# Performance work log

Hardware: AMD Instinct MI355X
Metric: run time of the kernel (lower is better)

## Reference

```python
import jax, jax.numpy as jnp
import numpy as np

B, S, D = 1, 2048, 4096
H = 32
HD = D // H  # 128
THETA = 10000.0


def _precompute_freqs_cis(dim, end, dtype=jnp.float32):
    freqs = 1.0 / THETA ** (jnp.arange(0, dim, 2)[: dim // 2].astype(dtype) / dim)
    t = jnp.arange(end)
    freqs = jnp.outer(t, freqs).astype(dtype)
    return jnp.complex64(jnp.cos(freqs) + 1j * jnp.sin(freqs))  # [end, dim//2]


def _apply_rotary_emb(xq, xk, freqs_cis, dtype=jnp.float32):
    # xq, xk: [b, s, h, hd]; freqs_cis: [1, s, hd//2] complex
    rq = xq.astype(jnp.float32).reshape(*xq.shape[:-1], -1, 2)
    rk = xk.astype(jnp.float32).reshape(*xk.shape[:-1], -1, 2)
    xq_ = jax.lax.complex(rq[..., 0], rq[..., 1])
    xk_ = jax.lax.complex(rk[..., 0], rk[..., 1])
    fc = jnp.reshape(freqs_cis, (*freqs_cis.shape[:2], 1, *freqs_cis.shape[2:]))  # [1,s,1,hd//2]
    xq_out = xq_ * fc
    xk_out = xk_ * fc
    xq_out = jnp.stack((jnp.real(xq_out), jnp.imag(xq_out)), axis=-1).reshape(*xq_out.shape[:-1], -1)
    xk_out = jnp.stack((jnp.real(xk_out), jnp.imag(xk_out)), axis=-1).reshape(*xk_out.shape[:-1], -1)
    return xq_out.astype(dtype), xk_out.astype(dtype)


def setup_inputs() -> dict:
    key = jax.random.key(0)
    k1, k2, k3 = jax.random.split(key, 3)
    scale = 1.0 / np.sqrt(D)
    return {
        "hidden_states": jax.random.normal(k1, (B, S, D), dtype=jnp.float32),
        "w_qkv_kernel": jax.random.normal(k2, (D, 3 * D), dtype=jnp.float32) * scale,
        "wo_kernel": jax.random.normal(k3, (D, D), dtype=jnp.float32) * scale,
    }


def reference(hidden_states, w_qkv_kernel, wo_kernel):
    b, s, d = hidden_states.shape
    qkv = hidden_states @ w_qkv_kernel  # [b, s, 3d]
    q, k, v = jnp.split(qkv, 3, -1)
    q = q.reshape(b, s, H, HD)
    k = k.reshape(b, s, H, HD)
    v = v.reshape(b, s, H, HD)
    freq = _precompute_freqs_cis(HD, S)[:s].reshape(1, s, -1)
    q, k = _apply_rotary_emb(q, k, freq)
    attn = jnp.einsum("bqhd,bkhd->bhqk", q, k)
    attn = attn * (1.0 / np.sqrt(HD))
    attn = jax.nn.softmax(attn, axis=-1)
    out = jnp.einsum("bhqk,bkhd->bqhd", attn, v).reshape(b, s, d)
    return out @ wo_kernel
```

## Files before the change

### kernel.cpp

```cpp
#include <hip/hip_runtime.h>
#include <cstdint>

#define S_LEN   2048
#define D_MODEL 4096
#define NHEAD   32
#define HDIM    128
#define LDQKV   12288

typedef __bf16 bf16x8 __attribute__((ext_vector_type(8)));
typedef float  f32x4  __attribute__((ext_vector_type(4)));
typedef unsigned short u16;
typedef unsigned int   u32;

union U16x8 { u16 u[8]; uint4 v; };

static __device__ __forceinline__ u16 f2b(float f) {
  u32 u = __builtin_bit_cast(u32, f);
  u += 0x7fffu + ((u >> 16) & 1u);
  return (u16)(u >> 16);
}
static __device__ __forceinline__ float b2f(u16 h) {
  u32 u = ((u32)h) << 16;
  return __builtin_bit_cast(float, u);
}

#define GLOAD_LDS16(gp, lp)                                                   \
  __builtin_amdgcn_global_load_lds(                                           \
      (const __attribute__((address_space(1))) unsigned int*)(gp),            \
      (__attribute__((address_space(3))) unsigned int*)(lp), 16, 0, 0)

__global__ __launch_bounds__(256) void convert_f32_bf16(
    const float* __restrict__ in, u16* __restrict__ out) {
  size_t i = (size_t)blockIdx.x * 256 + threadIdx.x;
  const float4* p = (const float4*)in;
  float4 a = p[2 * i], b = p[2 * i + 1];
  U16x8 r;
  r.u[0] = f2b(a.x); r.u[1] = f2b(a.y); r.u[2] = f2b(a.z); r.u[3] = f2b(a.w);
  r.u[4] = f2b(b.x); r.u[5] = f2b(b.y); r.u[6] = f2b(b.z); r.u[7] = f2b(b.w);
  *(uint4*)(out + 8 * i) = r.v;
}

__global__ __launch_bounds__(256) void tconv(
    const float* __restrict__ in, u16* __restrict__ out, int R, int C) {
  __shared__ __align__(16) u16 tile[64][72];
  const int r0 = blockIdx.y * 64, c0 = blockIdx.x * 64;
  const int tid = threadIdx.x;
  const int tr = tid >> 4, tc = (tid & 15) * 4;
#pragma unroll
  for (int p = 0; p < 4; ++p) {
    float4 v = *(const float4*)(in + (size_t)(r0 + p * 16 + tr) * C + c0 + tc);
    u16* t = &tile[p * 16 + tr][tc];
    t[0] = f2b(v.x); t[1] = f2b(v.y); t[2] = f2b(v.z); t[3] = f2b(v.w);
  }
  __syncthreads();
  const int oc = tid >> 3, os = (tid & 7) * 8;
#pragma unroll
  for (int p = 0; p < 2; ++p) {
    U16x8 u;
#pragma unroll
    for (int j = 0; j < 8; ++j) u.u[j] = tile[os + j][p * 32 + oc];
    *(uint4*)(out + (size_t)(c0 + p * 32 + oc) * R + r0 + os) = u.v;
  }
}

template <typename OutT>
__global__ __launch_bounds__(256) void gemm_bt(
    const u16* __restrict__ A, const u16* __restrict__ Bt, OutT* __restrict__ C,
    int M, int N, int K) {
  __shared__ __align__(16) u16 As[128 * 64];
  __shared__ __align__(16) u16 Bs[128 * 64];
  const int tid = threadIdx.x;
  const int lane = tid & 63, wave = tid >> 6;
  const int lane15 = lane & 15, quad = lane >> 4;
  const int wm = (wave >> 1) * 64, wn = (wave & 1) * 64;
  const size_t bm = (size_t)blockIdx.y * 128, bn = (size_t)blockIdx.x * 128;
  const int sreg_row = lane >> 3;
  const int schunk = lane & 7;

  f32x4 acc[4][4] = {};

  for (int k0 = 0; k0 < K; k0 += 64) {
#pragma unroll
    for (int i = 0; i < 4; ++i) {
      const int reg = wave * 4 + i;
      const int row = reg * 8 + sreg_row;
      const int gc = schunk ^ (row & 7);
      GLOAD_LDS16(A + (bm + row) * (size_t)K + k0 + gc * 8, &As[reg * 512]);
      GLOAD_LDS16(Bt + (bn + row) * (size_t)K + k0 + gc * 8, &Bs[reg * 512]);
    }
    __syncthreads();
#pragma unroll
    for (int kk = 0; kk < 64; kk += 32) {
      const int cb = kk >> 3;
      bf16x8 af[4], bfr[4];
#pragma unroll
      for (int mt = 0; mt < 4; ++mt) {
        const int row = wm + mt * 16 + lane15;
        af[mt] = *(const bf16x8*)&As[row * 64 + (((cb + quad) ^ (lane15 & 7)) * 8)];
      }
#pragma unroll
      for (int nt = 0; nt < 4; ++nt) {
        const int row = wn + nt * 16 + lane15;
        bfr[nt] = *(const bf16x8*)&Bs[row * 64 + (((cb + quad) ^ (lane15 & 7)) * 8)];
      }
#pragma unroll
      for (int mt = 0; mt < 4; ++mt)
#pragma unroll
        for (int nt = 0; nt < 4; ++nt)
          acc[mt][nt] = __builtin_amdgcn_mfma_f32_16x16x32_bf16(
              af[mt], bfr[nt], acc[mt][nt], 0, 0, 0);
    }
    __syncthreads();
  }
#pragma unroll
  for (int mt = 0; mt < 4; ++mt)
#pragma unroll
    for (int r = 0; r < 4; ++r) {
      size_t row = bm + wm + mt * 16 + quad * 4 + r;
#pragma unroll
      for (int nt = 0; nt < 4; ++nt) {
        size_t col = bn + wn + nt * 16 + lane15;
        float v = acc[mt][nt][r];
        if constexpr (sizeof(OutT) == 2) C[row * N + col] = (OutT)f2b(v);
        else                             C[row * N + col] = v;
      }
    }
}

__global__ __launch_bounds__(256) void rope_kernel(u16* __restrict__ qkv) {
  int idx = blockIdx.x * 256 + threadIdx.x;
  int s = idx >> 11;
  int p = idx & 2047;
  int h = p >> 6, j = p & 63;
  float freq = exp2f(-(float)j * 0.20762050593046015f);
  float ang = (float)s * freq;
  float sn, cs;
  sincosf(ang, &sn, &cs);
  size_t base = (size_t)s * LDQKV + h * HDIM + 2 * j;
  u32 q = *(const u32*)(qkv + base);
  float q0 = b2f((u16)(q & 0xffff)), q1 = b2f((u16)(q >> 16));
  u32 qo = (u32)f2b(q0 * cs - q1 * sn) | ((u32)f2b(q0 * sn + q1 * cs) << 16);
  *(u32*)(qkv + base) = qo;
  u32 k = *(const u32*)(qkv + base + D_MODEL);
  float k0 = b2f((u16)(k & 0xffff)), k1 = b2f((u16)(k >> 16));
  u32 ko = (u32)f2b(k0 * cs - k1 * sn) | ((u32)f2b(k0 * sn + k1 * cs) << 16);
  *(u32*)(qkv + base + D_MODEL) = ko;
}

__global__ __launch_bounds__(256) void transpose_v(
    const u16* __restrict__ qkv, u16* __restrict__ vt) {
  __shared__ __align__(16) u16 tile[64][72];
  const int s0 = blockIdx.x * 64, d0 = blockIdx.y * 64, h = blockIdx.z;
  const int tid = threadIdx.x;
  const int tr = tid >> 3, tc = (tid & 7) * 8;
#pragma unroll
  for (int p = 0; p < 2; ++p)
    *(uint4*)&tile[p * 32 + tr][tc] =
        *(const uint4*)(qkv + (size_t)(s0 + p * 32 + tr) * LDQKV + 2 * D_MODEL +
                        h * HDIM + d0 + tc);
  __syncthreads();
  const int dd = tid >> 3, ss = (tid & 7) * 8;
#pragma unroll
  for (int p = 0; p < 2; ++p) {
    U16x8 u;
#pragma unroll
    for (int j = 0; j < 8; ++j) u.u[j] = tile[ss + j][p * 32 + dd];
    *(uint4*)(vt + (size_t)h * HDIM * S_LEN + (size_t)(d0 + p * 32 + dd) * S_LEN +
              s0 + ss) = u.v;
  }
}

__global__ __launch_bounds__(256) void attn_kernel(
    const u16* __restrict__ qkv, const u16* __restrict__ vt, u16* __restrict__ ctx) {
  __shared__ __align__(16) u16 Ks[64 * 136];
  __shared__ __align__(16) u16 Vs[128 * 72];
  __shared__ __align__(16) u16 Ps[4][16 * 72];
  const int h = blockIdx.y, qt = blockIdx.x;
  const int tid = threadIdx.x;
  const int lane = tid & 63, wave = tid >> 6;
  const int lane15 = lane & 15, quad = lane >> 4;
  const int q0 = qt * 64 + wave * 16;

  bf16x8 aq[4];
#pragma unroll
  for (int kt = 0; kt < 4; ++kt)
    aq[kt] = *(const bf16x8*)(qkv + (size_t)(q0 + lane15) * LDQKV + h * HDIM +
                              kt * 32 + quad * 8);

  f32x4 o[8] = {};
  float lsum[4] = {0.f, 0.f, 0.f, 0.f};

  const int krow = tid >> 4, kcol = (tid & 15) * 8;
  const int vrow = tid >> 3, vcol = (tid & 7) * 8;
  const float cexp = 0.12751879523243985f;

  for (int kv0 = 0; kv0 < S_LEN; kv0 += 64) {
#pragma unroll
    for (int p = 0; p < 4; ++p)
      *(uint4*)&Ks[(p * 16 + krow) * 136 + kcol] =
          *(const uint4*)(qkv + (size_t)(kv0 + p * 16 + krow) * LDQKV + D_MODEL +
                          h * HDIM + kcol);
#pragma unroll
    for (int p = 0; p < 4; ++p)
      *(uint4*)&Vs[(p * 32 + vrow) * 72 + vcol] =
          *(const uint4*)(vt + (size_t)h * HDIM * S_LEN +
                          (size_t)(p * 32 + vrow) * S_LEN + kv0 + vcol);
    __syncthreads();

    f32x4 sf[4] = {};
#pragma unroll
    for (int nt = 0; nt < 4; ++nt)
#pragma unroll
      for (int kt = 0; kt < 4; ++kt) {
        bf16x8 bk = *(const bf16x8*)&Ks[(nt * 16 + lane15) * 136 + kt * 32 + quad * 8];
        sf[nt] = __builtin_amdgcn_mfma_f32_16x16x32_bf16(aq[kt], bk, sf[nt], 0, 0, 0);
      }

#pragma unroll
    for (int nt = 0; nt < 4; ++nt)
#pragma unroll
      for (int r = 0; r < 4; ++r) {
        float pv = exp2f(sf[nt][r] * cexp);
        lsum[r] += pv;
        Ps[wave][(quad * 4 + r) * 72 + nt * 16 + lane15] = f2b(pv);
      }

#pragma unroll
    for (int kt2 = 0; kt2 < 2; ++kt2) {
      bf16x8 ap = *(const bf16x8*)&Ps[wave][lane15 * 72 + kt2 * 32 + quad * 8];
#pragma unroll
      for (int nt2 = 0; nt2 < 8; ++nt2) {
        bf16x8 bv = *(const bf16x8*)&Vs[(nt2 * 16 + lane15) * 72 + kt2 * 32 + quad * 8];
        o[nt2] = __builtin_amdgcn_mfma_f32_16x16x32_bf16(ap, bv, o[nt2], 0, 0, 0);
      }
    }
    __syncthreads();
  }

#pragma unroll
  for (int r = 0; r < 4; ++r) {
    float l = lsum[r];
    l += __shfl_xor(l, 1);
    l += __shfl_xor(l, 2);
    l += __shfl_xor(l, 4);
    l += __shfl_xor(l, 8);
    float inv = 1.0f / l;
    size_t row = q0 + quad * 4 + r;
#pragma unroll
    for (int nt2 = 0; nt2 < 8; ++nt2)
      ctx[row * D_MODEL + h * HDIM + nt2 * 16 + lane15] = f2b(o[nt2][r] * inv);
  }
}

extern "C" void kernel_launch(void* const* d_in, const int* in_sizes, int n_in,
                              void* d_out, int out_size, void* d_ws, size_t ws_size,
                              hipStream_t stream) {
  const float* hs    = (const float*)d_in[0];
  const float* w_qkv = (const float*)d_in[1];
  const float* wo    = (const float*)d_in[2];
  float* out = (float*)d_out;

  char* w = (char*)d_ws;
  u16* hsb   = (u16*)(w);
  u16* wqkvT = (u16*)(w + (16u  << 20));
  u16* woT   = (u16*)(w + (112u << 20));
  u16* qkvb  = (u16*)(w + (144u << 20));
  u16* vt    = (u16*)(w + (192u << 20));
  u16* ctx   = hsb;

  convert_f32_bf16<<<4096, 256, 0, stream>>>(hs, hsb);
  tconv<<<dim3(12288 / 64, 4096 / 64), 256, 0, stream>>>(w_qkv, wqkvT, 4096, 12288);
  tconv<<<dim3(4096 / 64, 4096 / 64), 256, 0, stream>>>(wo, woT, 4096, 4096);

  gemm_bt<u16><<<dim3(12288 / 128, 2048 / 128), 256, 0, stream>>>(
      hsb, wqkvT, qkvb, 2048, 12288, 4096);

  rope_kernel<<<(S_LEN * 2048) / 256, 256, 0, stream>>>(qkvb);
  transpose_v<<<dim3(32, 2, 32), 256, 0, stream>>>(qkvb, vt);
  attn_kernel<<<dim3(32, 32), 256, 0, stream>>>(qkvb, vt, ctx);

  gemm_bt<float><<<dim3(4096 / 128, 2048 / 128), 256, 0, stream>>>(
      ctx, woT, out, 2048, 4096, 4096);
}
```

Measured before the change: 934.1 us.

## Double query rows per attention wave, use direct-to-LDS swizzled K/V loads

Each attention wave now processes 32 query rows instead of 16, so every K and V fragment read from LDS feeds two MFMAs, and the grid shrinks to 16x32 blocks. K/V tiles are loaded with global_load_lds into XOR-swizzled unpadded LDS layouts, which avoids register staging and bank conflicts. The transpose kernels switch to a 65-wide padded tile with scalar LDS writes, and rope uses fast __sinf/__cosf. Costs include higher register pressure, fewer blocks in flight, and reduced accuracy of sin/cos for large angles.

```diff
diff --git a/kernel.cpp b/kernel.cpp
--- a/kernel.cpp
+++ b/kernel.cpp
@@ -42,7 +42,7 @@
 
 __global__ __launch_bounds__(256) void tconv(
     const float* __restrict__ in, u16* __restrict__ out, int R, int C) {
-  __shared__ __align__(16) u16 tile[64][72];
+  __shared__ u16 tile[64][65];
   const int r0 = blockIdx.y * 64, c0 = blockIdx.x * 64;
   const int tid = threadIdx.x;
   const int tr = tid >> 4, tc = (tid & 15) * 4;
@@ -134,8 +134,7 @@
   int h = p >> 6, j = p & 63;
   float freq = exp2f(-(float)j * 0.20762050593046015f);
   float ang = (float)s * freq;
-  float sn, cs;
-  sincosf(ang, &sn, &cs);
+  float sn = __sinf(ang), cs = __cosf(ang);
   size_t base = (size_t)s * LDQKV + h * HDIM + 2 * j;
   u32 q = *(const u32*)(qkv + base);
   float q0 = b2f((u16)(q & 0xffff)), q1 = b2f((u16)(q >> 16));
@@ -149,15 +148,19 @@
 
 __global__ __launch_bounds__(256) void transpose_v(
     const u16* __restrict__ qkv, u16* __restrict__ vt) {
-  __shared__ __align__(16) u16 tile[64][72];
+  __shared__ u16 tile[64][65];
   const int s0 = blockIdx.x * 64, d0 = blockIdx.y * 64, h = blockIdx.z;
   const int tid = threadIdx.x;
   const int tr = tid >> 3, tc = (tid & 7) * 8;
 #pragma unroll
-  for (int p = 0; p < 2; ++p)
-    *(uint4*)&tile[p * 32 + tr][tc] =
-        *(const uint4*)(qkv + (size_t)(s0 + p * 32 + tr) * LDQKV + 2 * D_MODEL +
-                        h * HDIM + d0 + tc);
+  for (int p = 0; p < 2; ++p) {
+    U16x8 u;
+    u.v = *(const uint4*)(qkv + (size_t)(s0 + p * 32 + tr) * LDQKV + 2 * D_MODEL +
+                          h * HDIM + d0 + tc);
+    u16* t = &tile[p * 32 + tr][tc];
+#pragma unroll
+    for (int j = 0; j < 8; ++j) t[j] = u.u[j];
+  }
   __syncthreads();
   const int dd = tid >> 3, ss = (tid & 7) * 8;
 #pragma unroll
@@ -170,86 +173,106 @@
   }
 }
 
-__global__ __launch_bounds__(256) void attn_kernel(
+__global__ __launch_bounds__(256, 2) void attn_kernel(
     const u16* __restrict__ qkv, const u16* __restrict__ vt, u16* __restrict__ ctx) {
-  __shared__ __align__(16) u16 Ks[64 * 136];
-  __shared__ __align__(16) u16 Vs[128 * 72];
-  __shared__ __align__(16) u16 Ps[4][16 * 72];
+  __shared__ __align__(16) u16 Ks[64 * 128];
+  __shared__ __align__(16) u16 Vs[128 * 64];
+  __shared__ __align__(16) u16 Ps[4][32 * 72];
   const int h = blockIdx.y, qt = blockIdx.x;
   const int tid = threadIdx.x;
   const int lane = tid & 63, wave = tid >> 6;
   const int lane15 = lane & 15, quad = lane >> 4;
-  const int q0 = qt * 64 + wave * 16;
-
-  bf16x8 aq[4];
-#pragma unroll
-  for (int kt = 0; kt < 4; ++kt)
-    aq[kt] = *(const bf16x8*)(qkv + (size_t)(q0 + lane15) * LDQKV + h * HDIM +
-                              kt * 32 + quad * 8);
-
-  f32x4 o[8] = {};
-  float lsum[4] = {0.f, 0.f, 0.f, 0.f};
-
-  const int krow = tid >> 4, kcol = (tid & 15) * 8;
-  const int vrow = tid >> 3, vcol = (tid & 7) * 8;
+  const int q0 = qt * 128 + wave * 32;
+
+  bf16x8 aq[2][4];
+#pragma unroll
+  for (int mi = 0; mi < 2; ++mi)
+#pragma unroll
+    for (int kt = 0; kt < 4; ++kt)
+      aq[mi][kt] = *(const bf16x8*)(qkv + (size_t)(q0 + mi * 16 + lane15) * LDQKV +
+                                    h * HDIM + kt * 32 + quad * 8);
+
+  f32x4 o[2][8] = {};
+  float lsum[2][4] = {};
+
+  const int krow_off = wave * 16 + (lane >> 4);
+  const int kslot = lane & 15;
+  const int vrow_off = wave * 32 + (lane >> 3);
+  const int vslot = lane & 7;
+  const u16* kbase = qkv + D_MODEL + h * HDIM;
+  const u16* vbase = vt + (size_t)h * HDIM * S_LEN;
   const float cexp = 0.12751879523243985f;
 
   for (int kv0 = 0; kv0 < S_LEN; kv0 += 64) {
 #pragma unroll
-    for (int p = 0; p < 4; ++p)
-      *(uint4*)&Ks[(p * 16 + krow) * 136 + kcol] =
-          *(const uint4*)(qkv + (size_t)(kv0 + p * 16 + krow) * LDQKV + D_MODEL +
-                          h * HDIM + kcol);
-#pragma unroll
-    for (int p = 0; p < 4; ++p)
-      *(uint4*)&Vs[(p * 32 + vrow) * 72 + vcol] =
-          *(const uint4*)(vt + (size_t)h * HDIM * S_LEN +
-                          (size_t)(p * 32 + vrow) * S_LEN + kv0 + vcol);
+    for (int i = 0; i < 4; ++i) {
+      const int krow = krow_off + i * 4;
+      const int kgc = kslot ^ (krow & 7);
+      GLOAD_LDS16(kbase + (size_t)(kv0 + krow) * LDQKV + kgc * 8,
+                  &Ks[(wave * 16 + i * 4) * 128]);
+      const int vrow = vrow_off + i * 8;
+      const int vgc = vslot ^ (vrow & 7);
+      GLOAD_LDS16(vbase + (size_t)vrow * S_LEN + kv0 + vgc * 8,
+                  &Vs[(wave * 32 + i * 8) * 64]);
+    }
     __syncthreads();
 
-    f32x4 sf[4] = {};
-#pragma unroll
-    for (int nt = 0; nt < 4; ++nt)
+    f32x4 sf[2][4] = {};
+#pragma unroll
+    for (int nt = 0; nt < 4; ++nt) {
+      bf16x8 bk[4];
+#pragma unroll
+      for (int kt = 0; kt < 4; ++kt)
+        bk[kt] = *(const bf16x8*)&Ks[(nt * 16 + lane15) * 128 +
+                                     (((kt * 4 + quad) ^ (lane15 & 7)) * 8)];
 #pragma unroll
       for (int kt = 0; kt < 4; ++kt) {
-        bf16x8 bk = *(const bf16x8*)&Ks[(nt * 16 + lane15) * 136 + kt * 32 + quad * 8];
-        sf[nt] = __builtin_amdgcn_mfma_f32_16x16x32_bf16(aq[kt], bk, sf[nt], 0, 0, 0);
-      }
-
-#pragma unroll
-    for (int nt = 0; nt < 4; ++nt)
-#pragma unroll
-      for (int r = 0; r < 4; ++r) {
-        float pv = exp2f(sf[nt][r] * cexp);
-        lsum[r] += pv;
-        Ps[wave][(quad * 4 + r) * 72 + nt * 16 + lane15] = f2b(pv);
-      }
+        sf[0][nt] = __builtin_amdgcn_mfma_f32_16x16x32_bf16(aq[0][kt], bk[kt], sf[0][nt], 0, 0, 0);
+        sf[1][nt] = __builtin_amdgcn_mfma_f32_16x16x32_bf16(aq[1][kt], bk[kt], sf[1][nt], 0, 0, 0);
+      }
+    }
+
+#pragma unroll
+    for (int mi = 0; mi < 2; ++mi)
+#pragma unroll
+      for (int nt = 0; nt < 4; ++nt)
+#pragma unroll
+        for (int r = 0; r < 4; ++r) {
+          float pv = exp2f(sf[mi][nt][r] * cexp);
+          lsum[mi][r] += pv;
+          Ps[wave][(mi * 16 + quad * 4 + r) * 72 + nt * 16 + lane15] = f2b(pv);
+        }
 
 #pragma unroll
     for (int kt2 = 0; kt2 < 2; ++kt2) {
-      bf16x8 ap = *(const bf16x8*)&Ps[wave][lane15 * 72 + kt2 * 32 + quad * 8];
+      bf16x8 ap0 = *(const bf16x8*)&Ps[wave][(lane15) * 72 + kt2 * 32 + quad * 8];
+      bf16x8 ap1 = *(const bf16x8*)&Ps[wave][(16 + lane15) * 72 + kt2 * 32 + quad * 8];
 #pragma unroll
       for (int nt2 = 0; nt2 < 8; ++nt2) {
-        bf16x8 bv = *(const bf16x8*)&Vs[(nt2 * 16 + lane15) * 72 + kt2 * 32 + quad * 8];
-        o[nt2] = __builtin_amdgcn_mfma_f32_16x16x32_bf16(ap, bv, o[nt2], 0, 0, 0);
+        bf16x8 bv = *(const bf16x8*)&Vs[(nt2 * 16 + lane15) * 64 +
+                                        (((kt2 * 4 + quad) ^ (lane15 & 7)) * 8)];
+        o[0][nt2] = __builtin_amdgcn_mfma_f32_16x16x32_bf16(ap0, bv, o[0][nt2], 0, 0, 0);
+        o[1][nt2] = __builtin_amdgcn_mfma_f32_16x16x32_bf16(ap1, bv, o[1][nt2], 0, 0, 0);
       }
     }
     __syncthreads();
   }
 
 #pragma unroll
-  for (int r = 0; r < 4; ++r) {
-    float l = lsum[r];
-    l += __shfl_xor(l, 1);
-    l += __shfl_xor(l, 2);
-    l += __shfl_xor(l, 4);
-    l += __shfl_xor(l, 8);
-    float inv = 1.0f / l;
-    size_t row = q0 + quad * 4 + r;
-#pragma unroll
-    for (int nt2 = 0; nt2 < 8; ++nt2)
-      ctx[row * D_MODEL + h * HDIM + nt2 * 16 + lane15] = f2b(o[nt2][r] * inv);
-  }
+  for (int mi = 0; mi < 2; ++mi)
+#pragma unroll
+    for (int r = 0; r < 4; ++r) {
+      float l = lsum[mi][r];
+      l += __shfl_xor(l, 1);
+      l += __shfl_xor(l, 2);
+      l += __shfl_xor(l, 4);
+      l += __shfl_xor(l, 8);
+      float inv = 1.0f / l;
+      size_t row = q0 + mi * 16 + quad * 4 + r;
+#pragma unroll
+      for (int nt2 = 0; nt2 < 8; ++nt2)
+        ctx[row * D_MODEL + h * HDIM + nt2 * 16 + lane15] = f2b(o[mi][nt2][r] * inv);
+    }
 }
 
 extern "C" void kernel_launch(void* const* d_in, const int* in_sizes, int n_in,
@@ -277,7 +300,7 @@
 
   rope_kernel<<<(S_LEN * 2048) / 256, 256, 0, stream>>>(qkvb);
   transpose_v<<<dim3(32, 2, 32), 256, 0, stream>>>(qkvb, vt);
-  attn_kernel<<<dim3(32, 32), 256, 0, stream>>>(qkvb, vt, ctx);
+  attn_kernel<<<dim3(16, 32), 256, 0, stream>>>(qkvb, vt, ctx);
 
   gemm_bt<float><<<dim3(4096 / 128, 2048 / 128), 256, 0, stream>>>(
       ctx, woT, out, 2048, 4096, 4096);
```

New measurement: 772.0 us. 1.21x faster.
